# Kernel tuning notes

Measured on AMD Instinct MI355X. Metric: run time of the kernel, lower is better.

Reference implementation:

```python
import jax, jax.numpy as jnp
import numpy as np

N = 100_000   # nodes
E = 3_200_000 # edges (avg degree 32)
K = 10        # propagation hops


def setup_inputs() -> dict:
    key = jax.random.key(0)
    ks = jax.random.split(key, 9)
    x = jax.random.normal(ks[0], (N, 1), dtype=jnp.float32)
    edge_index = jax.random.randint(ks[1], (2, E), 0, N, dtype=jnp.int32)
    # MLP params (lin1: 1->32, lin2: 32->64, fc2: 64->1)
    W1 = jax.random.normal(ks[2], (1, 32), dtype=jnp.float32) * 0.5
    b1 = jnp.zeros((32,), dtype=jnp.float32)
    W2 = jax.random.normal(ks[3], (32, 64), dtype=jnp.float32) * (1.0 / np.sqrt(32))
    b2 = jnp.zeros((64,), dtype=jnp.float32)
    # GPR temp coefficients, Init='Random': uniform(-b, b), b=sqrt(3/(K+1)), L1-normalized
    bound = float(np.sqrt(3.0 / (K + 1)))
    temp = jax.random.uniform(ks[4], (K + 1,), dtype=jnp.float32,
                              minval=-bound, maxval=bound)
    temp = temp / jnp.sum(jnp.abs(temp))
    W_fc = jax.random.normal(ks[5], (64, 1), dtype=jnp.float32) * (1.0 / np.sqrt(64))
    b_fc = jnp.zeros((1,), dtype=jnp.float32)
    return {"x": x, "edge_index": edge_index, "W1": W1, "b1": b1,
            "W2": W2, "b2": b2, "temp": temp, "W_fc": W_fc, "b_fc": b_fc}


def reference(x, edge_index, W1, b1, W2, b2, temp, W_fc, b_fc):
    n = x.shape[0]
    # feature MLP
    h = jax.nn.relu(x @ W1 + b1)       # [N, 32]
    h = jax.nn.relu(h @ W2 + b2)       # [N, 64]
    # gcn_norm with self-loops, edge_weight = 1
    loops = jnp.arange(n, dtype=edge_index.dtype)
    row = jnp.concatenate([edge_index[0], loops])  # source
    col = jnp.concatenate([edge_index[1], loops])  # target (aggregation index)
    ones = jnp.ones(row.shape, dtype=h.dtype)
    deg = jax.ops.segment_sum(ones, col, num_segments=n)
    dinv = jnp.where(deg > 0, jax.lax.rsqrt(deg), 0.0)
    norm = dinv[row] * dinv[col]       # [E+N]
    # K-hop GPR propagation: hidden = sum_k temp[k] * A_hat^k h
    hidden0 = temp[0] * h

    def step(carry, gamma):
        xc, hid = carry
        msg = norm[:, None] * xc[row]                       # gather + scale
        xn = jax.ops.segment_sum(msg, col, num_segments=n)  # scatter-add
        return (xn, hid + gamma * xn), None

    (_, hidden), _ = jax.lax.scan(step, (h, hidden0), temp[1:])
    return hidden @ W_fc + b_fc        # [N, 1]
```

## Files before the change

kernel.cpp:

```cpp
#include <hip/hip_runtime.h>


#define TPB  256
#define SBSH 10
#define CAP1 37376
#define EPT  16
#define CH   (TPB * EPT)

__global__ void k_zero(int* __restrict__ bcursor, int nsb) {
    int i = blockIdx.x * blockDim.x + threadIdx.x;
    if (i < nsb) bcursor[i] = 0;
}

__global__ void k_scatter(const int* __restrict__ erow, const int* __restrict__ ecol,
                          int* __restrict__ bcursor, unsigned int* __restrict__ ebuf1,
                          const float* __restrict__ x, const float* __restrict__ W1,
                          const float* __restrict__ b1, const float* __restrict__ W2,
                          const float* __restrict__ b2, const float* __restrict__ Wfc,
                          float* __restrict__ zarr, int e, int n, int nsb) {
    __shared__ int hist[128];
    __shared__ int base[128];
    int t = threadIdx.x;
    int s = blockIdx.x * CH;
    int r[EPT], c[EPT];

    if (t < 128) hist[t] = 0;
    __syncthreads();
#pragma unroll
    for (int j = 0; j < EPT; j++) {
        int i = s + j * TPB + t;
        bool ok = (i < e);
        c[j] = ok ? ecol[i] : -1;
        r[j] = ok ? erow[i] : 0;
        if (ok) atomicAdd(&hist[c[j] >> SBSH], 1);
    }
    __syncthreads();
    if (t < nsb) {
        int cc = hist[t];
        base[t] = cc ? atomicAdd(&bcursor[t], cc) : 0;
        hist[t] = 0;
    }
    __syncthreads();
#pragma unroll
    for (int j = 0; j < EPT; j++) {
        if (c[j] >= 0) {
            int b = c[j] >> SBSH;
            int pos = base[b] + atomicAdd(&hist[b], 1);
            if (pos < CAP1)
                ebuf1[(size_t)b * CAP1 + pos] =
                    ((unsigned int)r[j] << SBSH) | (unsigned int)(c[j] & ((1 << SBSH) - 1));
        }
    }

    int gw = (blockIdx.x * TPB + t) >> 6;
    int nwaves = (gridDim.x * TPB) >> 6;
    int lane = t & 63;
    float b2l = b2[lane];
    float wfl = Wfc[lane];
    for (int node = gw; node < n; node += nwaves) {
        float xv = x[node];
        float acc = b2l;
#pragma unroll
        for (int j = 0; j < 32; j++) {
            float h1 = fmaxf(fmaf(xv, W1[j], b1[j]), 0.f);
            acc = fmaf(h1, W2[j * 64 + lane], acc);
        }
        float cz = fmaxf(acc, 0.f) * wfl;
#pragma unroll
        for (int o = 32; o >= 1; o >>= 1) cz += __shfl_xor(cz, o);
        if (lane == 0) zarr[node] = cz;
    }
}

__global__ void __launch_bounds__(1024)
k_sub(const int* __restrict__ bcursor, const unsigned int* __restrict__ ebuf1,
      unsigned int* __restrict__ csr, int2* __restrict__ rs_re,
      float2* __restrict__ nrm, const float* __restrict__ zarr,
      const float* __restrict__ temp, const float* __restrict__ bfc,
      float* __restrict__ u0, float* __restrict__ u1,
      float* __restrict__ out, int n) {
    __shared__ int hist[1024];
    __shared__ int wsum[16];
    int b = blockIdx.x;
    int t = threadIdx.x;
    int lane = t & 63;
    int w = t >> 6;

    hist[t] = 0;
    __syncthreads();
    int cnt = min(bcursor[b], CAP1);
    size_t g = (size_t)b * CAP1;
    int last = cnt > 0 ? cnt - 1 : 0;
    for (int j = t; j < cnt; j += 4096) {
        int j1 = j + 1024, j2 = j + 2048, j3 = j + 3072;
        unsigned int p0 = ebuf1[g + j];
        unsigned int p1 = ebuf1[g + min(j1, last)];
        unsigned int p2 = ebuf1[g + min(j2, last)];
        unsigned int p3 = ebuf1[g + min(j3, last)];
        atomicAdd(&hist[p0 & 1023], 1);
        if (j1 < cnt) atomicAdd(&hist[p1 & 1023], 1);
        if (j2 < cnt) atomicAdd(&hist[p2 & 1023], 1);
        if (j3 < cnt) atomicAdd(&hist[p3 & 1023], 1);
    }
    __syncthreads();

    int deg = hist[t];
    int pdeg = (deg + 3) & ~3;
    int v = pdeg;
#pragma unroll
    for (int o = 1; o < 64; o <<= 1) {
        int u = __shfl_up(v, o);
        if (lane >= o) v += u;
    }
    if (lane == 63) wsum[w] = v;
    __syncthreads();
    if (w == 0) {
        int sv = (lane < 16) ? wsum[lane] : 0;
#pragma unroll
        for (int o = 1; o < 16; o <<= 1) {
            int u = __shfl_up(sv, o);
            if (lane >= o) sv += u;
        }
        if (lane < 16) wsum[lane] = sv;
    }
    __syncthreads();
    int pexcl = v - pdeg + (w > 0 ? wsum[w - 1] : 0);

    int node = (b << SBSH) + t;
    if (node < n) {
        int bs = (int)g + pexcl;
        rs_re[node] = make_int2(bs, bs + pdeg);
        float d = (float)(deg + 1);
        float di = rsqrtf(d);
        nrm[node] = make_float2(di * di, d * di);
        float z = zarr[node];
        u0[node] = di * z;
        out[node] = fmaf(temp[0], z, bfc[0]);
    }
    if (b == 0 && t == 0) { u0[n] = 0.f; u1[n] = 0.f; }
    __syncthreads();
    hist[t] = pexcl;
    __syncthreads();
    for (int j = t; j < cnt; j += 4096) {
        int j1 = j + 1024, j2 = j + 2048, j3 = j + 3072;
        unsigned int p0 = ebuf1[g + j];
        unsigned int p1 = ebuf1[g + min(j1, last)];
        unsigned int p2 = ebuf1[g + min(j2, last)];
        unsigned int p3 = ebuf1[g + min(j3, last)];
        int pos0 = atomicAdd(&hist[p0 & 1023], 1);
        csr[g + pos0] = p0 >> SBSH;
        if (j1 < cnt) { int p = atomicAdd(&hist[p1 & 1023], 1); csr[g + p] = p1 >> SBSH; }
        if (j2 < cnt) { int p = atomicAdd(&hist[p2 & 1023], 1); csr[g + p] = p2 >> SBSH; }
        if (j3 < cnt) { int p = atomicAdd(&hist[p3 & 1023], 1); csr[g + p] = p3 >> SBSH; }
    }
    __syncthreads();
    for (int p = pexcl + deg; p < pexcl + pdeg; p++)
        csr[g + p] = (unsigned int)n;
}

__global__ void k_hop(const int2* __restrict__ rs_re, const uint4* __restrict__ csr4,
                      const float2* __restrict__ nrm,
                      const float* __restrict__ uprev, float* __restrict__ ucur,
                      float* __restrict__ out, const float* __restrict__ temp,
                      int k, int n, int is_last) {
    int tid = blockIdx.x * blockDim.x + threadIdx.x;
    int node = tid >> 3;
    int sub = tid & 7;
    if (node >= n) return;
    int2 se = rs_re[node];
    int s4 = se.x >> 2;
    int e4 = se.y >> 2;
    float sum = (sub == 0) ? uprev[node] : 0.f;
    for (int i4 = s4 + sub; i4 < e4; i4 += 8) {
        uint4 a = csr4[i4];
        float v0 = uprev[a.x];
        float v1 = uprev[a.y];
        float v2 = uprev[a.z];
        float v3 = uprev[a.w];
        sum += (v0 + v1) + (v2 + v3);
    }
    sum += __shfl_xor(sum, 1);
    sum += __shfl_xor(sum, 2);
    sum += __shfl_xor(sum, 4);
    if (sub == 0) {
        float2 nv = nrm[node];
        float u = nv.x * sum;
        if (!is_last) ucur[node] = u;
        out[node] = fmaf(temp[k] * nv.y, u, out[node]);
    }
}

static inline size_t align256(size_t v) { return (v + 255) & ~(size_t)255; }

extern "C" void kernel_launch(void* const* d_in, const int* in_sizes, int n_in,
                              void* d_out, int out_size, void* d_ws, size_t ws_size,
                              hipStream_t stream) {
    const float* x    = (const float*)d_in[0];
    const int*   ei   = (const int*)d_in[1];
    const float* W1   = (const float*)d_in[2];
    const float* b1   = (const float*)d_in[3];
    const float* W2   = (const float*)d_in[4];
    const float* b2   = (const float*)d_in[5];
    const float* temp = (const float*)d_in[6];
    const float* Wfc  = (const float*)d_in[7];
    const float* bfc  = (const float*)d_in[8];

    const int n = in_sizes[0];
    const int e = in_sizes[1] / 2;
    const int K = in_sizes[6] - 1;
    const int nsb = (n + (1 << SBSH) - 1) >> SBSH;

    const int* erow = ei;
    const int* ecol = ei + e;

    float* out = (float*)d_out;

    char* ws = (char*)d_ws;
    int*          bcursor = (int*)ws;          ws += align256((size_t)128 * 4);
    unsigned int* ebuf1   = (unsigned int*)ws; ws += align256((size_t)nsb * CAP1 * 4);
    unsigned int* csr     = (unsigned int*)ws; ws += align256((size_t)nsb * CAP1 * 4);
    int2*         rs_re   = (int2*)ws;         ws += align256((size_t)n * 8);
    float2*       nrm     = (float2*)ws;       ws += align256((size_t)n * 8);
    float*        zarr    = (float*)ws;        ws += align256((size_t)(n + 1) * 4);
    float*        u0      = (float*)ws;        ws += align256((size_t)(n + 1) * 4);
    float*        u1      = (float*)ws;        ws += align256((size_t)(n + 1) * 4);

    const int gS = (e + CH - 1) / CH;
    const int gH = (8 * n + TPB - 1) / TPB;

    k_zero<<<1, 128, 0, stream>>>(bcursor, nsb);
    k_scatter<<<gS, TPB, 0, stream>>>(erow, ecol, bcursor, ebuf1,
                                      x, W1, b1, W2, b2, Wfc, zarr, e, n, nsb);
    k_sub<<<nsb, 1024, 0, stream>>>(bcursor, ebuf1, csr, rs_re, nrm,
                                    zarr, temp, bfc, u0, u1, out, n);

    float* uin = u0;
    float* uout = u1;
    for (int k = 1; k <= K; k++) {
        k_hop<<<gH, TPB, 0, stream>>>(rs_re, (const uint4*)csr, nrm, uin, uout,
                                      out, temp, k, n, (k == K) ? 1 : 0);
        float* t2 = uin; uin = uout; uout = t2;
    }
}
```

Measured before the change: 334.6 us.

## Split MLP into per-node-thread kernel fused with cursor zeroing, widen scatter blocks

```diff
diff --git a/kernel.cpp b/kernel.cpp
--- a/kernel.cpp
+++ b/kernel.cpp
@@ -2,22 +2,48 @@
 
 
 #define TPB  256
+#define TSC  512
 #define SBSH 10
 #define CAP1 37376
-#define EPT  16
-#define CH   (TPB * EPT)
-
-__global__ void k_zero(int* __restrict__ bcursor, int nsb) {
+#define EPT  8
+#define CH   (TSC * EPT)
+
+__global__ void k_mlp(const float* __restrict__ x, const float* __restrict__ W1,
+                      const float* __restrict__ b1, const float* __restrict__ W2,
+                      const float* __restrict__ b2, const float* __restrict__ Wfc,
+                      float* __restrict__ zarr, int* __restrict__ bcursor, int n) {
     int i = blockIdx.x * blockDim.x + threadIdx.x;
-    if (i < nsb) bcursor[i] = 0;
-}
-
-__global__ void k_scatter(const int* __restrict__ erow, const int* __restrict__ ecol,
-                          int* __restrict__ bcursor, unsigned int* __restrict__ ebuf1,
-                          const float* __restrict__ x, const float* __restrict__ W1,
-                          const float* __restrict__ b1, const float* __restrict__ W2,
-                          const float* __restrict__ b2, const float* __restrict__ Wfc,
-                          float* __restrict__ zarr, int e, int n, int nsb) {
+    if (i < 128) bcursor[i] = 0;
+    if (i >= n) return;
+    float xv = x[i];
+    float h1[32];
+#pragma unroll
+    for (int j = 0; j < 32; j++)
+        h1[j] = fmaxf(fmaf(xv, W1[j], b1[j]), 0.f);
+    float z = 0.f;
+#pragma unroll
+    for (int fc = 0; fc < 4; fc++) {
+        float acc[16];
+#pragma unroll
+        for (int f = 0; f < 16; f++) acc[f] = b2[fc * 16 + f];
+#pragma unroll
+        for (int j = 0; j < 32; j++) {
+            float h = h1[j];
+#pragma unroll
+            for (int f = 0; f < 16; f++)
+                acc[f] = fmaf(h, W2[j * 64 + fc * 16 + f], acc[f]);
+        }
+#pragma unroll
+        for (int f = 0; f < 16; f++)
+            z = fmaf(fmaxf(acc[f], 0.f), Wfc[fc * 16 + f], z);
+    }
+    zarr[i] = z;
+}
+
+__global__ void __launch_bounds__(TSC)
+k_scatter(const int* __restrict__ erow, const int* __restrict__ ecol,
+          int* __restrict__ bcursor, unsigned int* __restrict__ ebuf1,
+          int e, int nsb) {
     __shared__ int hist[128];
     __shared__ int base[128];
     int t = threadIdx.x;
@@ -28,7 +54,7 @@
     __syncthreads();
 #pragma unroll
     for (int j = 0; j < EPT; j++) {
-        int i = s + j * TPB + t;
+        int i = s + j * TSC + t;
         bool ok = (i < e);
         c[j] = ok ? ecol[i] : -1;
         r[j] = ok ? erow[i] : 0;
@@ -48,27 +74,8 @@
             int pos = base[b] + atomicAdd(&hist[b], 1);
             if (pos < CAP1)
                 ebuf1[(size_t)b * CAP1 + pos] =
-                    ((unsigned int)r[j] << SBSH) | (unsigned int)(c[j] & ((1 << SBSH) - 1));
+                    ((unsigned int)r[j] << SBSH) | (unsigned int)(c[j] & 1023);
         }
-    }
-
-    int gw = (blockIdx.x * TPB + t) >> 6;
-    int nwaves = (gridDim.x * TPB) >> 6;
-    int lane = t & 63;
-    float b2l = b2[lane];
-    float wfl = Wfc[lane];
-    for (int node = gw; node < n; node += nwaves) {
-        float xv = x[node];
-        float acc = b2l;
-#pragma unroll
-        for (int j = 0; j < 32; j++) {
-            float h1 = fmaxf(fmaf(xv, W1[j], b1[j]), 0.f);
-            acc = fmaf(h1, W2[j * 64 + lane], acc);
-        }
-        float cz = fmaxf(acc, 0.f) * wfl;
-#pragma unroll
-        for (int o = 32; o >= 1; o >>= 1) cz += __shfl_xor(cz, o);
-        if (lane == 0) zarr[node] = cz;
     }
 }
 
@@ -225,12 +232,12 @@
     float*        u0      = (float*)ws;        ws += align256((size_t)(n + 1) * 4);
     float*        u1      = (float*)ws;        ws += align256((size_t)(n + 1) * 4);
 
+    const int gM = (n + TPB - 1) / TPB;
     const int gS = (e + CH - 1) / CH;
     const int gH = (8 * n + TPB - 1) / TPB;
 
-    k_zero<<<1, 128, 0, stream>>>(bcursor, nsb);
-    k_scatter<<<gS, TPB, 0, stream>>>(erow, ecol, bcursor, ebuf1,
-                                      x, W1, b1, W2, b2, Wfc, zarr, e, n, nsb);
+    k_mlp<<<gM, TPB, 0, stream>>>(x, W1, b1, W2, b2, Wfc, zarr, bcursor, n);
+    k_scatter<<<gS, TSC, 0, stream>>>(erow, ecol, bcursor, ebuf1, e, nsb);
     k_sub<<<nsb, 1024, 0, stream>>>(bcursor, ebuf1, csr, rs_re, nrm,
                                     zarr, temp, bfc, u0, u1, out, n);
 
```

Result: no change. 332.2 us (median of 2 runs) (-0.7%).
